# Performance work log

Measured on AMD Instinct MI355X. Metric: run time of the kernel, lower is better.

## Reference

```python
import jax, jax.numpy as jnp
import numpy as np

N = 50000      # neurons
R = 4          # receptors per neuron
D = 5          # max delay steps
N_IN = 17400   # input (LGN) channels
B = 2
T = 50
E_REC = 2000000
E_IN = 500000
DT = 1.0
SIGMA = 0.5    # gauss_std
DAMP = 0.3     # dampening_factor


@jax.custom_vjp
def spike_gauss(v):
    return (v > 0).astype(v.dtype)

def _sg_fwd(v):
    return (v > 0).astype(v.dtype), v

def _sg_bwd(v, g):
    return (g * jnp.exp(-(v * v) / (SIGMA * SIGMA)) * DAMP,)

spike_gauss.defvjp(_sg_fwd, _sg_bwd)


def _constrained(w):
    # Dale's law: sign buffer is fixed (stop_gradient), values clipped to keep sign
    s = jax.lax.stop_gradient(jnp.sign(w))
    return jnp.where(s >= 0, jax.nn.relu(w), -jax.nn.relu(-w))


def setup_inputs() -> dict:
    ks = jax.random.split(jax.random.key(0), 20)
    x = jax.random.uniform(ks[0], (B, T, N_IN), jnp.float32)
    rest = jax.random.randint(ks[1], (T, B), 0, 11).astype(jnp.int32)  # Binomial(10,0.1) count
    rec_rows = jax.random.randint(ks[2], (E_REC,), 0, R * N).astype(jnp.int32)
    rec_cols = jax.random.randint(ks[3], (E_REC,), 0, D * N).astype(jnp.int32)
    rec_w = jax.random.normal(ks[4], (E_REC,), jnp.float32) * 1e-3
    in_rows = jax.random.randint(ks[5], (E_IN,), 0, R * N).astype(jnp.int32)
    in_cols = jax.random.randint(ks[6], (E_IN,), 0, N_IN).astype(jnp.int32)
    in_w = jax.random.normal(ks[7], (E_IN,), jnp.float32) * 1e-3
    bkg = jax.random.normal(ks[8], (N * R,), jnp.float32) * 0.1
    # per-neuron params, already in normalized voltage units (offset=E_L, scale=V_th-E_L)
    v_th = jnp.ones((N,), jnp.float32)
    e_l = jnp.zeros((N,), jnp.float32)
    v_reset = jax.random.uniform(ks[9], (N,), jnp.float32, -0.2, 0.0)
    g = jax.random.uniform(ks[10], (N,), jnp.float32, 4.0, 6.0)
    c_m = jax.random.uniform(ks[11], (N,), jnp.float32, 100.0, 200.0)
    tau = c_m / g
    decay = jnp.exp(-DT / tau)
    current_factor = (1.0 - decay) * tau / c_m
    t_ref = jnp.full((N,), 2.0, jnp.float32)
    asc_amps = jax.random.normal(ks[12], (N, 2), jnp.float32) * 0.01
    param_k = jax.random.uniform(ks[13], (N, 2), jnp.float32, 0.1, 0.5)
    tau_syn = jax.random.uniform(ks[14], (N, R), jnp.float32, 2.0, 10.0)
    syn_decay = jnp.exp(-DT / tau_syn)
    psc_initial = jnp.asarray(np.e, jnp.float32) / tau_syn
    voltage_scale = jax.random.uniform(ks[15], (N,), jnp.float32, 20.0, 30.0)
    voltage_offset = jnp.full((N,), -70.0, jnp.float32)
    return dict(x=x, rec_w=rec_w, in_w=in_w, bkg=bkg, v_th=v_th, e_l=e_l,
                v_reset=v_reset, g=g, t_ref=t_ref, asc_amps=asc_amps,
                param_k=param_k, decay=decay, current_factor=current_factor,
                syn_decay=syn_decay, psc_initial=psc_initial,
                voltage_scale=voltage_scale, voltage_offset=voltage_offset,
                rec_rows=rec_rows, rec_cols=rec_cols, in_rows=in_rows,
                in_cols=in_cols, rest=rest)


def _forward(x, rec_w, in_w, bkg, v_th, e_l, v_reset, g, t_ref, asc_amps,
             param_k, decay, current_factor, syn_decay, psc_initial,
             voltage_scale, voltage_offset, rec_rows, rec_cols, in_rows,
             in_cols, rest):
    rec_wc = _constrained(rec_w)
    in_wc = _constrained(in_w)
    asc_decay = jnp.exp(-DT * param_k)   # (N,2)
    leak = g * e_l                       # (N,)
    normalizer = v_th - e_l              # (N,)

    z_buf0 = jnp.zeros((B, D, N), jnp.float32)  # delay line, slot 0 = most recent
    v0 = jnp.broadcast_to(v_reset, (B, N))
    zN = jnp.zeros((B, N), jnp.float32)
    zNR = jnp.zeros((B, N, R), jnp.float32)
    carry0 = (z_buf0, v0, zN, zN, zN, zNR, zNR)

    xs = (jnp.transpose(x, (1, 0, 2)), rest)  # (T,B,N_IN), (T,B)

    def step(carry, inp):
        x_t, rest_t = inp
        z_buf, v, r, a1, a2, psc_rise, psc = carry
        # input projection: sparse COO (R*N, N_IN) matvec per batch via gather + scatter-add
        cur = jnp.zeros((B, R * N), jnp.float32).at[:, in_rows].add(x_t[:, in_cols] * in_wc[None, :])
        cur = cur + bkg[None, :] * (rest_t.astype(jnp.float32)[:, None] / 10.0)
        prev_z = z_buf[:, 0]
        zb_flat = z_buf.reshape(B, D * N)
        # recurrent sparse COO (R*N, D*N) matvec over the delay buffer
        i_rec = jnp.zeros((B, R * N), jnp.float32).at[:, rec_rows].add(zb_flat[:, rec_cols] * rec_wc[None, :])
        rec_in = (i_rec + cur).reshape(B, N, R)
        new_psc_rise = syn_decay[None] * psc_rise + rec_in * psc_initial[None]
        new_psc = psc * syn_decay[None] + DT * syn_decay[None] * psc_rise
        new_r = jax.nn.relu(r + prev_z * t_ref[None] - DT)
        new_a1 = asc_decay[:, 0][None] * a1 + prev_z * asc_amps[:, 0][None]
        new_a2 = asc_decay[:, 1][None] * a2 + prev_z * asc_amps[:, 1][None]
        reset_current = prev_z * (v_reset - v_th)[None]
        input_current = psc.sum(-1)  # uses OLD psc, matching the torch code
        new_v = decay[None] * v + current_factor[None] * (input_current + a1 + a2 + leak[None]) + reset_current
        v_sc = (new_v - v_th[None]) / normalizer[None]
        new_z = spike_gauss(v_sc)
        new_z = jnp.where(new_r > 0.0, jnp.zeros_like(new_z), new_z)
        new_z_buf = jnp.concatenate([new_z[:, None, :], z_buf[:, :-1]], axis=1)
        v_out = new_v * voltage_scale[None] + voltage_offset[None]
        new_carry = (new_z_buf, new_v, new_r, new_a1, new_a2, new_psc_rise, new_psc)
        return new_carry, (new_z, v_out)

    _, (zs, vs) = jax.lax.scan(step, carry0, xs)
    return jnp.transpose(zs, (1, 0, 2)), jnp.transpose(vs, (1, 0, 2))  # (B,T,N) each


def reference(x, rec_w, in_w, bkg, v_th, e_l, v_reset, g, t_ref, asc_amps,
              param_k, decay, current_factor, syn_decay, psc_initial,
              voltage_scale, voltage_offset, rec_rows, rec_cols, in_rows,
              in_cols, rest):
    return _forward(x, rec_w, in_w, bkg, v_th, e_l, v_reset, g, t_ref,
                    asc_amps, param_k, decay, current_factor, syn_decay,
                    psc_initial, voltage_scale, voltage_offset, rec_rows,
                    rec_cols, in_rows, in_cols, rest)
```

## Files before the change

kernel.cpp:

```cpp
#include <hip/hip_runtime.h>
#include <hip/hip_cooperative_groups.h>

namespace cg = cooperative_groups;

#define NN    50000
#define RR    4
#define DDEP  5
#define NIN   17400
#define BB    2
#define TT    50
#define EREC  2000000
#define EIN   500000
#define RNN   (RR*NN)
#define DNN   (DDEP*NN)
#define RING  6
#define TB    (TT*BB)
#define CH    20
#define NCH   (TB/CH)
#define SCAN_TPB 256
#define SCAN_ITEMS 4

struct SP {
  const float* x; const float* bkg;
  const float* v_th; const float* e_l; const float* v_reset; const float* g;
  const float* t_ref; const float* asc_amps; const float* param_k;
  const float* decay; const float* cf; const float* syn_decay; const float* psc_init;
  const float* vscale; const float* voff;
  const int* rest;
  float* out_z; float* out_v;
  float* cur_ring;
  int*   flags;
  int*   bar;
  const int* row_ptr;
  const int2* cw_in;
  const int* col_ptr;
  const int2* cw_rec;
  const float* in_cur;
};

__global__ void hist2_k(const int* __restrict__ in_rows, const int* __restrict__ rec_cols,
                        int* __restrict__ cnt_in, int* __restrict__ cnt_rec) {
  int i = blockIdx.x * blockDim.x + threadIdx.x;
  int nth = gridDim.x * blockDim.x;
  for (int e = i; e < EIN + EREC; e += nth) {
    if (e < EIN) atomicAdd(&cnt_in[in_rows[e]], 1);
    else         atomicAdd(&cnt_rec[rec_cols[e - EIN]], 1);
  }
}

__global__ __launch_bounds__(SCAN_TPB) void blocksum_k(const int* __restrict__ cnt, int n,
                                                       int* __restrict__ partial) {
  __shared__ int sm[SCAN_TPB];
  int base = (blockIdx.x * SCAN_TPB + threadIdx.x) * SCAN_ITEMS;
  int s = 0;
  #pragma unroll
  for (int j = 0; j < SCAN_ITEMS; ++j) { int idx = base + j; if (idx < n) s += cnt[idx]; }
  sm[threadIdx.x] = s; __syncthreads();
  for (int off = SCAN_TPB / 2; off > 0; off >>= 1) {
    if (threadIdx.x < off) sm[threadIdx.x] += sm[threadIdx.x + off];
    __syncthreads();
  }
  if (threadIdx.x == 0) partial[blockIdx.x] = sm[0];
}

__global__ __launch_bounds__(SCAN_TPB) void scanpart_k(int* __restrict__ partial, int nb) {
  __shared__ int sm[SCAN_TPB];
  int i = threadIdx.x;
  int v = (i < nb) ? partial[i] : 0;
  sm[i] = v; __syncthreads();
  for (int off = 1; off < SCAN_TPB; off <<= 1) {
    int a = (i >= off) ? sm[i - off] : 0;
    __syncthreads();
    sm[i] += a;
    __syncthreads();
  }
  if (i < nb) partial[i] = sm[i] - v;
}

__global__ __launch_bounds__(SCAN_TPB) void finalize_k(const int* __restrict__ cnt, int n,
                                                       const int* __restrict__ partial,
                                                       int* __restrict__ ptr,
                                                       int* __restrict__ cursor, int nE) {
  __shared__ int sm[SCAN_TPB];
  int tidl = threadIdx.x;
  int base = (blockIdx.x * SCAN_TPB + tidl) * SCAN_ITEMS;
  int local[SCAN_ITEMS];
  int s = 0;
  #pragma unroll
  for (int j = 0; j < SCAN_ITEMS; ++j) {
    int idx = base + j;
    int c = (idx < n) ? cnt[idx] : 0;
    local[j] = c; s += c;
  }
  sm[tidl] = s; __syncthreads();
  for (int off = 1; off < SCAN_TPB; off <<= 1) {
    int a = (tidl >= off) ? sm[tidl - off] : 0;
    __syncthreads();
    sm[tidl] += a;
    __syncthreads();
  }
  int run = partial[blockIdx.x] + sm[tidl] - s;
  #pragma unroll
  for (int j = 0; j < SCAN_ITEMS; ++j) {
    int idx = base + j;
    if (idx < n) { ptr[idx] = run; cursor[idx] = run; run += local[j]; }
  }
  if (blockIdx.x == 0 && tidl == 0) ptr[n] = nE;
}

__global__ void scatter2_k(const int* __restrict__ in_rows, const int* __restrict__ in_cols,
                           const float* __restrict__ in_w,
                           const int* __restrict__ rec_cols, const int* __restrict__ rec_rows,
                           const float* __restrict__ rec_w,
                           int* __restrict__ cur_in, int* __restrict__ cur_rec,
                           int2* __restrict__ cw_in, int2* __restrict__ cw_rec) {
  int i = blockIdx.x * blockDim.x + threadIdx.x;
  int nth = gridDim.x * blockDim.x;
  for (int e = i; e < EIN + EREC; e += nth) {
    if (e < EIN) {
      int pos = atomicAdd(&cur_in[in_rows[e]], 1);
      cw_in[pos] = make_int2(in_cols[e], __float_as_int(in_w[e]));
    } else {
      int ee = e - EIN;
      int pos = atomicAdd(&cur_rec[rec_cols[ee]], 1);
      cw_rec[pos] = make_int2(rec_rows[ee], __float_as_int(rec_w[ee]));
    }
  }
}

__global__ __launch_bounds__(256) void xpose_k(const float* __restrict__ x,
                                               float* __restrict__ xT) {
  __shared__ float tile[64][TB + 1];
  int c0 = blockIdx.x * 64;
  int cl = threadIdx.x & 63;
  for (int tb = threadIdx.x >> 6; tb < TB; tb += 4) {
    int t = tb >> 1, b = tb & 1;
    int c = c0 + cl;
    tile[cl][tb] = (c < NIN) ? x[((size_t)b * TT + t) * NIN + c] : 0.f;
  }
  __syncthreads();
  int cc = threadIdx.x >> 2;
  int seg = (threadIdx.x & 3) * (TB / 4);
  int c = c0 + cc;
  if (c < NIN) {
    for (int j = seg; j < seg + TB / 4; ++j)
      xT[(size_t)c * TB + j] = tile[cc][j];
  }
}

__global__ __launch_bounds__(256) void precomp2_k(const float* __restrict__ xT,
                                                  const int* __restrict__ rest,
                                                  const float* __restrict__ bkg,
                                                  const int* __restrict__ row_ptr,
                                                  const int2* __restrict__ cw,
                                                  float* __restrict__ ic) {
  const int nbn = (NN + 255) >> 8;
  int chunk = blockIdx.x / nbn;
  int n = (blockIdx.x % nbn) * 256 + threadIdx.x;
  if (n >= NN) return;
  const int tb0 = chunk * CH;

  float restf[CH];
  #pragma unroll
  for (int j = 0; j < CH; ++j) restf[j] = (float)rest[tb0 + j] * 0.1f;

  int rp[RR + 1];
  #pragma unroll
  for (int r = 0; r <= RR; ++r) rp[r] = row_ptr[n * RR + r];

  float acc[RR][CH];
  #pragma unroll
  for (int r = 0; r < RR; ++r) {
    float bk = bkg[n * RR + r];
    #pragma unroll
    for (int j = 0; j < CH; ++j) acc[r][j] = bk * restf[j];
    for (int e = rp[r]; e < rp[r + 1]; ++e) {
      int2 c = cw[e];
      float w = __int_as_float(c.y);
      const float* xr = xT + (size_t)c.x * TB + tb0;
      #pragma unroll
      for (int j = 0; j < CH; ++j) acc[r][j] += w * xr[j];
    }
  }
  #pragma unroll
  for (int j = 0; j < CH; ++j) {
    *(float4*)(ic + (size_t)(tb0 + j) * RNN + (size_t)n * RR) =
        make_float4(acc[0][j], acc[1][j], acc[2][j], acc[3][j]);
  }
}

__device__ __forceinline__ void gridbar(int* bar, int nb, int target) {
  __syncthreads();
  if (threadIdx.x == 0) {
    int* cnt = bar;
    int* gen = bar + 32;
    int old = __hip_atomic_fetch_add(cnt, 1, __ATOMIC_ACQ_REL, __HIP_MEMORY_SCOPE_AGENT);
    if (old == nb - 1) {
      __hip_atomic_store(cnt, 0, __ATOMIC_RELAXED, __HIP_MEMORY_SCOPE_AGENT);
      __hip_atomic_store(gen, target, __ATOMIC_RELEASE, __HIP_MEMORY_SCOPE_AGENT);
    } else {
      while (__hip_atomic_load(gen, __ATOMIC_RELAXED, __HIP_MEMORY_SCOPE_AGENT) < target)
        __builtin_amdgcn_s_sleep(2);
      (void)__hip_atomic_load(gen, __ATOMIC_ACQUIRE, __HIP_MEMORY_SCOPE_AGENT);
    }
  }
  __syncthreads();
}

__global__ __launch_bounds__(1024, 1) void snn_all(SP p) {
  const int tid = blockIdx.x * blockDim.x + threadIdx.x;
  const int nb = gridDim.x;

  const bool owner = tid < BB * NN;
  int b = 0, n = 0;
  float sd[RR], pi[RR], bkgv[RR], psc_rise[RR], psc[RR];
  int rbeg[RR], rend[RR];
  float v = 0.f, refr = 0.f, a1 = 0.f, a2 = 0.f, my_z = 0.f;
  float dcy = 0.f, cfac = 0.f, trf = 0.f, amp1 = 0.f, amp2 = 0.f;
  float ad1 = 0.f, ad2 = 0.f, vth = 0.f, invn = 0.f, leak = 0.f;
  float vrst = 0.f, vsc = 0.f, vof = 0.f;
  #pragma unroll
  for (int r = 0; r < RR; ++r) {
    sd[r]=0.f; pi[r]=0.f; bkgv[r]=0.f; psc_rise[r]=0.f; psc[r]=0.f;
    rbeg[r]=0; rend[r]=0;
  }

  if (owner) {
    b = (tid >= NN) ? 1 : 0;
    n = tid - b * NN;
    #pragma unroll
    for (int r = 0; r < RR; ++r) {
      sd[r] = p.syn_decay[n*RR + r];
      pi[r] = p.psc_init[n*RR + r];
    }
    if (!p.in_cur) {
      #pragma unroll
      for (int r = 0; r < RR; ++r) {
        bkgv[r] = p.bkg[n*RR + r];
        rbeg[r] = p.row_ptr[n*RR + r];
        rend[r] = p.row_ptr[n*RR + r + 1];
      }
    }
    vth  = p.v_th[n];
    float el = p.e_l[n];
    invn = 1.0f / (vth - el);
    leak = p.g[n] * el;
    vrst = p.v_reset[n];
    v    = vrst;
    dcy  = p.decay[n];
    cfac = p.cf[n];
    trf  = p.t_ref[n];
    amp1 = p.asc_amps[2*n+0];
    amp2 = p.asc_amps[2*n+1];
    ad1  = expf(-p.param_k[2*n+0]);
    ad2  = expf(-p.param_k[2*n+1]);
    vsc  = p.vscale[n];
    vof  = p.voff[n];
  }
  const float* xb = p.x + (size_t)b * TT * NIN;
  float* ringB = p.cur_ring + (size_t)b * RING * RNN;

  float4 iv = make_float4(0.f, 0.f, 0.f, 0.f);
  if (owner && p.in_cur)
    iv = *(const float4*)(p.in_cur + (size_t)b * RNN + (size_t)n * RR);

  for (int t = 0; t < TT; ++t) {
    if (t) gridbar(p.bar, nb, t);

    if (owner) {
      int slot = t % RING;
      float rin[RR];

      if (p.in_cur) {
        rin[0] = iv.x; rin[1] = iv.y; rin[2] = iv.z; rin[3] = iv.w;
      } else {
        float restf = (float)p.rest[t*BB + b] * 0.1f;
        const float* xt = xb + (size_t)t * NIN;
        #pragma unroll
        for (int r = 0; r < RR; ++r) {
          float acc = bkgv[r] * restf;
          for (int e = rbeg[r]; e < rend[r]; ++e) {
            int2 cw = p.cw_in[e];
            acc += xt[cw.x] * __int_as_float(cw.y);
          }
          rin[r] = acc;
        }
      }

      if (p.flags[b*RING + slot] == t) {
        float4* slotR = (float4*)(ringB + (size_t)slot * RNN);
        float4 rv = slotR[n];
        slotR[n] = make_float4(0.f, 0.f, 0.f, 0.f);
        rin[0] += rv.x; rin[1] += rv.y; rin[2] += rv.z; rin[3] += rv.w;
      }

      float prev_z = my_z;
      float input_current = psc[0] + psc[1] + psc[2] + psc[3];
      float new_v = dcy * v + cfac * (input_current + a1 + a2 + leak)
                    + prev_z * (vrst - vth);
      #pragma unroll
      for (int r = 0; r < RR; ++r) {
        float npsc = psc[r] * sd[r] + sd[r] * psc_rise[r];
        psc_rise[r] = sd[r] * psc_rise[r] + rin[r] * pi[r];
        psc[r] = npsc;
      }
      refr = fmaxf(refr + prev_z * trf - 1.0f, 0.f);
      a1 = ad1 * a1 + prev_z * amp1;
      a2 = ad2 * a2 + prev_z * amp2;
      v = new_v;
      float v_scaled = (new_v - vth) * invn;
      float z = (v_scaled > 0.f) ? 1.f : 0.f;
      if (refr > 0.f) z = 0.f;
      my_z = z;
      size_t oidx = (size_t)b * (TT*NN) + (size_t)t * NN + n;
      p.out_z[oidx] = z;
      p.out_v[oidx] = new_v * vsc + vof;

      if (z != 0.f) {
        #pragma unroll
        for (int d = 0; d < DDEP; ++d) {
          int tt = t + 1 + d;
          if (tt >= TT) break;
          int col = d * NN + n;
          int be = p.col_ptr[col], en = p.col_ptr[col + 1];
          if (be != en) {
            int ws_ = tt % RING;
            p.flags[b*RING + ws_] = tt;
            float* ringW = ringB + (size_t)ws_ * RNN;
            for (int e = be; e < en; ++e) {
              int2 cw = p.cw_rec[e];
              atomicAdd(&ringW[cw.x], __int_as_float(cw.y));
            }
          }
        }
      }

      if (p.in_cur && t + 1 < TT)
        iv = *(const float4*)(p.in_cur + (size_t)((t+1)*BB + b) * RNN + (size_t)n * RR);
    }
  }
}

extern "C" void kernel_launch(void* const* d_in, const int* in_sizes, int n_in,
                              void* d_out, int out_size, void* d_ws, size_t ws_size,
                              hipStream_t stream) {
  SP p;
  p.x        = (const float*)d_in[0];
  const float* rec_w = (const float*)d_in[1];
  const float* in_w  = (const float*)d_in[2];
  p.bkg      = (const float*)d_in[3];
  p.v_th     = (const float*)d_in[4];
  p.e_l      = (const float*)d_in[5];
  p.v_reset  = (const float*)d_in[6];
  p.g        = (const float*)d_in[7];
  p.t_ref    = (const float*)d_in[8];
  p.asc_amps = (const float*)d_in[9];
  p.param_k  = (const float*)d_in[10];
  p.decay    = (const float*)d_in[11];
  p.cf       = (const float*)d_in[12];
  p.syn_decay= (const float*)d_in[13];
  p.psc_init = (const float*)d_in[14];
  p.vscale   = (const float*)d_in[15];
  p.voff     = (const float*)d_in[16];
  const int* rec_rows = (const int*)d_in[17];
  const int* rec_cols = (const int*)d_in[18];
  const int* in_rows  = (const int*)d_in[19];
  const int* in_cols  = (const int*)d_in[20];
  p.rest     = (const int*)d_in[21];
  p.out_z = (float*)d_out;
  p.out_v = (float*)d_out + (size_t)BB * TT * NN;

  char* ws = (char*)d_ws;
  size_t off = 0;
  auto alloc = [&](size_t bytes) { void* q = ws + off; off += (bytes + 255) & ~(size_t)255; return q; };
  float* cur_ring = (float*)alloc(sizeof(float) * (size_t)BB * RING * RNN);
  int*   flags    = (int*)  alloc(sizeof(int) * BB * RING);
  int*   bar      = (int*)  alloc(sizeof(int) * 64);
  int*   row_ptr  = (int*)  alloc(sizeof(int) * ((size_t)RNN + 1));
  int*   col_ptr  = (int*)  alloc(sizeof(int) * ((size_t)DNN + 1));
  int*   cnt_in   = (int*)  alloc(sizeof(int) * (size_t)RNN);
  int*   cnt_rec  = (int*)  alloc(sizeof(int) * (size_t)DNN);
  int*   cur_in   = (int*)  alloc(sizeof(int) * (size_t)RNN);
  int*   cur_rec  = (int*)  alloc(sizeof(int) * (size_t)DNN);
  int*   part_in  = (int*)  alloc(sizeof(int) * SCAN_TPB);
  int*   part_rec = (int*)  alloc(sizeof(int) * SCAN_TPB);
  int2*  cw_in    = (int2*) alloc(sizeof(int2) * (size_t)EIN);
  int2*  cw_rec   = (int2*) alloc(sizeof(int2) * (size_t)EREC);
  float* xT       = (float*)alloc(sizeof(float) * (size_t)NIN * TB);
  float* in_cur   = (float*)alloc(sizeof(float) * (size_t)TB * RNN);
  const bool use_pre = (off <= ws_size);

  p.cur_ring = cur_ring; p.flags = flags; p.bar = bar;
  p.row_ptr = row_ptr; p.cw_in = cw_in;
  p.col_ptr = col_ptr; p.cw_rec = cw_rec;
  p.in_cur = use_pre ? in_cur : nullptr;

  hipMemsetAsync(cur_ring, 0, sizeof(float) * (size_t)BB * RING * RNN, stream);
  hipMemsetAsync(flags, 0xFF, sizeof(int) * BB * RING, stream);
  hipMemsetAsync(bar, 0, sizeof(int) * 64, stream);
  hipMemsetAsync(cnt_in, 0, sizeof(int) * (size_t)RNN, stream);
  hipMemsetAsync(cnt_rec, 0, sizeof(int) * (size_t)DNN, stream);

  hipLaunchKernelGGL(hist2_k, dim3(1024), dim3(256), 0, stream,
                     in_rows, rec_cols, cnt_in, cnt_rec);

  const int NB_IN  = (RNN + SCAN_TPB * SCAN_ITEMS - 1) / (SCAN_TPB * SCAN_ITEMS);
  const int NB_REC = (DNN + SCAN_TPB * SCAN_ITEMS - 1) / (SCAN_TPB * SCAN_ITEMS);
  hipLaunchKernelGGL(blocksum_k, dim3(NB_IN),  dim3(SCAN_TPB), 0, stream, cnt_in,  RNN, part_in);
  hipLaunchKernelGGL(blocksum_k, dim3(NB_REC), dim3(SCAN_TPB), 0, stream, cnt_rec, DNN, part_rec);
  hipLaunchKernelGGL(scanpart_k, dim3(1), dim3(SCAN_TPB), 0, stream, part_in,  NB_IN);
  hipLaunchKernelGGL(scanpart_k, dim3(1), dim3(SCAN_TPB), 0, stream, part_rec, NB_REC);
  hipLaunchKernelGGL(finalize_k, dim3(NB_IN),  dim3(SCAN_TPB), 0, stream, cnt_in,  RNN, part_in,  row_ptr, cur_in,  EIN);
  hipLaunchKernelGGL(finalize_k, dim3(NB_REC), dim3(SCAN_TPB), 0, stream, cnt_rec, DNN, part_rec, col_ptr, cur_rec, EREC);

  hipLaunchKernelGGL(scatter2_k, dim3(1024), dim3(256), 0, stream,
                     in_rows, in_cols, in_w, rec_cols, rec_rows, rec_w,
                     cur_in, cur_rec, cw_in, cw_rec);

  if (use_pre) {
    hipLaunchKernelGGL(xpose_k, dim3((NIN + 63) / 64), dim3(256), 0, stream, p.x, xT);
    const int nbn = (NN + 255) / 256;
    hipLaunchKernelGGL(precomp2_k, dim3(nbn * NCH), dim3(256), 0, stream,
                       xT, p.rest, p.bkg, row_ptr, cw_in, in_cur);
  }

  void* args[] = { (void*)&p };
  hipLaunchCooperativeKernel(reinterpret_cast<const void*>(&snn_all),
                             dim3(104), dim3(1024), args, 0u, stream);
}
```

Baseline: 835.1 us.

## Overlap input-current precompute with recurrent scan using helper blocks and tree barrier

Removes the separate precompute kernel and moves its work into the persistent cooperative kernel. Blocks beyond the first 98 act as helpers: they compute the first 20 time-batch slices before the first grid barrier, then compute two slices per step ahead of the owner blocks. The grid grows to 256 blocks and the flat grid barrier becomes a two-level tree barrier, which reduces contention on a single counter. The ring-slot flags are dropped in favour of an unconditional read-and-clear, the scan kernels are merged into paired launches, and the memsets are coalesced into one. The risks are a larger cooperative grid, extra traffic competing with the latency-bound step loop, and a barrier that now has more participants.

```diff
diff --git a/kernel.cpp b/kernel.cpp
--- a/kernel.cpp
+++ b/kernel.cpp
@@ -1,7 +1,4 @@
 #include <hip/hip_runtime.h>
-#include <hip/hip_cooperative_groups.h>
-
-namespace cg = cooperative_groups;
 
 #define NN    50000
 #define RR    4
@@ -15,8 +12,13 @@
 #define DNN   (DDEP*NN)
 #define RING  6
 #define TB    (TT*BB)
-#define CH    20
-#define NCH   (TB/CH)
+#define NBLK  256
+#define TPB   1024
+#define OWNER_BLKS 98
+#define NHELP ((NBLK-OWNER_BLKS)*TPB)
+#define GRP   16
+#define NGRP  (NBLK/GRP)
+#define PRE_SLICES 20
 #define SCAN_TPB 256
 #define SCAN_ITEMS 4
 
@@ -29,13 +31,14 @@
   const int* rest;
   float* out_z; float* out_v;
   float* cur_ring;
-  int*   flags;
   int*   bar;
   const int* row_ptr;
   const int2* cw_in;
   const int* col_ptr;
   const int2* cw_rec;
-  const float* in_cur;
+  const float* xT;
+  float* ic;
+  int    use_pre;
 };
 
 __global__ void hist2_k(const int* __restrict__ in_rows, const int* __restrict__ rec_cols,
@@ -48,8 +51,15 @@
   }
 }
 
-__global__ __launch_bounds__(SCAN_TPB) void blocksum_k(const int* __restrict__ cnt, int n,
-                                                       int* __restrict__ partial) {
+__global__ __launch_bounds__(SCAN_TPB) void blocksum2_k(const int* __restrict__ cnt_in,
+                                                        const int* __restrict__ cnt_rec,
+                                                        int* __restrict__ part_in,
+                                                        int* __restrict__ part_rec) {
+  const int n = blockIdx.y ? DNN : RNN;
+  const int* cnt = blockIdx.y ? cnt_rec : cnt_in;
+  int* partial = blockIdx.y ? part_rec : part_in;
+  const int nb = (n + SCAN_TPB * SCAN_ITEMS - 1) / (SCAN_TPB * SCAN_ITEMS);
+  if ((int)blockIdx.x >= nb) return;
   __shared__ int sm[SCAN_TPB];
   int base = (blockIdx.x * SCAN_TPB + threadIdx.x) * SCAN_ITEMS;
   int s = 0;
@@ -63,7 +73,11 @@
   if (threadIdx.x == 0) partial[blockIdx.x] = sm[0];
 }
 
-__global__ __launch_bounds__(SCAN_TPB) void scanpart_k(int* __restrict__ partial, int nb) {
+__global__ __launch_bounds__(SCAN_TPB) void scanpart2_k(int* __restrict__ part_in,
+                                                        int* __restrict__ part_rec) {
+  const int n = blockIdx.x ? DNN : RNN;
+  int* partial = blockIdx.x ? part_rec : part_in;
+  const int nb = (n + SCAN_TPB * SCAN_ITEMS - 1) / (SCAN_TPB * SCAN_ITEMS);
   __shared__ int sm[SCAN_TPB];
   int i = threadIdx.x;
   int v = (i < nb) ? partial[i] : 0;
@@ -77,10 +91,22 @@
   if (i < nb) partial[i] = sm[i] - v;
 }
 
-__global__ __launch_bounds__(SCAN_TPB) void finalize_k(const int* __restrict__ cnt, int n,
-                                                       const int* __restrict__ partial,
-                                                       int* __restrict__ ptr,
-                                                       int* __restrict__ cursor, int nE) {
+__global__ __launch_bounds__(SCAN_TPB) void finalize2_k(const int* __restrict__ cnt_in,
+                                                        const int* __restrict__ cnt_rec,
+                                                        const int* __restrict__ part_in,
+                                                        const int* __restrict__ part_rec,
+                                                        int* __restrict__ ptr_in,
+                                                        int* __restrict__ ptr_rec,
+                                                        int* __restrict__ cur_in,
+                                                        int* __restrict__ cur_rec) {
+  const int n = blockIdx.y ? DNN : RNN;
+  const int nE = blockIdx.y ? EREC : EIN;
+  const int* cnt = blockIdx.y ? cnt_rec : cnt_in;
+  const int* partial = blockIdx.y ? part_rec : part_in;
+  int* ptr = blockIdx.y ? ptr_rec : ptr_in;
+  int* cursor = blockIdx.y ? cur_rec : cur_in;
+  const int nb = (n + SCAN_TPB * SCAN_ITEMS - 1) / (SCAN_TPB * SCAN_ITEMS);
+  if ((int)blockIdx.x >= nb) return;
   __shared__ int sm[SCAN_TPB];
   int tidl = threadIdx.x;
   int base = (blockIdx.x * SCAN_TPB + tidl) * SCAN_ITEMS;
@@ -148,70 +174,53 @@
   }
 }
 
-__global__ __launch_bounds__(256) void precomp2_k(const float* __restrict__ xT,
-                                                  const int* __restrict__ rest,
-                                                  const float* __restrict__ bkg,
-                                                  const int* __restrict__ row_ptr,
-                                                  const int2* __restrict__ cw,
-                                                  float* __restrict__ ic) {
-  const int nbn = (NN + 255) >> 8;
-  int chunk = blockIdx.x / nbn;
-  int n = (blockIdx.x % nbn) * 256 + threadIdx.x;
-  if (n >= NN) return;
-  const int tb0 = chunk * CH;
-
-  float restf[CH];
-  #pragma unroll
-  for (int j = 0; j < CH; ++j) restf[j] = (float)rest[tb0 + j] * 0.1f;
-
-  int rp[RR + 1];
-  #pragma unroll
-  for (int r = 0; r <= RR; ++r) rp[r] = row_ptr[n * RR + r];
-
-  float acc[RR][CH];
-  #pragma unroll
-  for (int r = 0; r < RR; ++r) {
-    float bk = bkg[n * RR + r];
-    #pragma unroll
-    for (int j = 0; j < CH; ++j) acc[r][j] = bk * restf[j];
-    for (int e = rp[r]; e < rp[r + 1]; ++e) {
-      int2 c = cw[e];
-      float w = __int_as_float(c.y);
-      const float* xr = xT + (size_t)c.x * TB + tb0;
-      #pragma unroll
-      for (int j = 0; j < CH; ++j) acc[r][j] += w * xr[j];
-    }
-  }
-  #pragma unroll
-  for (int j = 0; j < CH; ++j) {
-    *(float4*)(ic + (size_t)(tb0 + j) * RNN + (size_t)n * RR) =
-        make_float4(acc[0][j], acc[1][j], acc[2][j], acc[3][j]);
-  }
-}
-
-__device__ __forceinline__ void gridbar(int* bar, int nb, int target) {
+__device__ __forceinline__ void gridbar(int* bar, int target) {
   __syncthreads();
   if (threadIdx.x == 0) {
-    int* cnt = bar;
-    int* gen = bar + 32;
-    int old = __hip_atomic_fetch_add(cnt, 1, __ATOMIC_ACQ_REL, __HIP_MEMORY_SCOPE_AGENT);
-    if (old == nb - 1) {
-      __hip_atomic_store(cnt, 0, __ATOMIC_RELAXED, __HIP_MEMORY_SCOPE_AGENT);
-      __hip_atomic_store(gen, target, __ATOMIC_RELEASE, __HIP_MEMORY_SCOPE_AGENT);
+    int* leaf = bar + (blockIdx.x / GRP) * 32;
+    int* rootGen = bar + NGRP * 32;
+    int* rootCnt = rootGen + 32;
+    int lo = __hip_atomic_fetch_add(leaf, 1, __ATOMIC_ACQ_REL, __HIP_MEMORY_SCOPE_AGENT);
+    if (lo == GRP - 1) {
+      __hip_atomic_store(leaf, 0, __ATOMIC_RELAXED, __HIP_MEMORY_SCOPE_AGENT);
+      int ro = __hip_atomic_fetch_add(rootCnt, 1, __ATOMIC_ACQ_REL, __HIP_MEMORY_SCOPE_AGENT);
+      if (ro == NGRP - 1) {
+        __hip_atomic_store(rootCnt, 0, __ATOMIC_RELAXED, __HIP_MEMORY_SCOPE_AGENT);
+        __hip_atomic_store(rootGen, target, __ATOMIC_RELEASE, __HIP_MEMORY_SCOPE_AGENT);
+      } else {
+        while (__hip_atomic_load(rootGen, __ATOMIC_RELAXED, __HIP_MEMORY_SCOPE_AGENT) < target)
+          __builtin_amdgcn_s_sleep(2);
+        (void)__hip_atomic_load(rootGen, __ATOMIC_ACQUIRE, __HIP_MEMORY_SCOPE_AGENT);
+      }
     } else {
-      while (__hip_atomic_load(gen, __ATOMIC_RELAXED, __HIP_MEMORY_SCOPE_AGENT) < target)
+      while (__hip_atomic_load(rootGen, __ATOMIC_RELAXED, __HIP_MEMORY_SCOPE_AGENT) < target)
         __builtin_amdgcn_s_sleep(2);
-      (void)__hip_atomic_load(gen, __ATOMIC_ACQUIRE, __HIP_MEMORY_SCOPE_AGENT);
+      (void)__hip_atomic_load(rootGen, __ATOMIC_ACQUIRE, __HIP_MEMORY_SCOPE_AGENT);
     }
   }
   __syncthreads();
 }
 
-__global__ __launch_bounds__(1024, 1) void snn_all(SP p) {
-  const int tid = blockIdx.x * blockDim.x + threadIdx.x;
-  const int nb = gridDim.x;
-
-  const bool owner = tid < BB * NN;
+__device__ __forceinline__ void helper_item(const SP& p, int n, int s) {
+  float restf = (float)p.rest[s] * 0.1f;
+  const int* rp = p.row_ptr + n * RR;
+  int r0 = rp[0], r1 = rp[1], r2 = rp[2], r3 = rp[3], r4 = rp[4];
+  float4 bk = *(const float4*)(p.bkg + (size_t)n * RR);
+  float a0 = bk.x * restf, a1 = bk.y * restf, a2 = bk.z * restf, a3 = bk.w * restf;
+  const float* xs = p.xT + s;
+  for (int e = r0; e < r1; ++e) { int2 c = p.cw_in[e]; a0 += __int_as_float(c.y) * xs[(size_t)c.x * TB]; }
+  for (int e = r1; e < r2; ++e) { int2 c = p.cw_in[e]; a1 += __int_as_float(c.y) * xs[(size_t)c.x * TB]; }
+  for (int e = r2; e < r3; ++e) { int2 c = p.cw_in[e]; a2 += __int_as_float(c.y) * xs[(size_t)c.x * TB]; }
+  for (int e = r3; e < r4; ++e) { int2 c = p.cw_in[e]; a3 += __int_as_float(c.y) * xs[(size_t)c.x * TB]; }
+  *(float4*)(p.ic + (size_t)s * RNN + (size_t)n * RR) = make_float4(a0, a1, a2, a3);
+}
+
+__global__ __launch_bounds__(TPB, 1) void snn_all(SP p) {
+  const int tid = blockIdx.x * TPB + threadIdx.x;
+  const bool hblk = blockIdx.x >= OWNER_BLKS;
+  const int hr = hblk ? (blockIdx.x - OWNER_BLKS) * TPB + threadIdx.x : 0;
+
+  const bool owner = !hblk && tid < BB * NN;
   int b = 0, n = 0;
   float sd[RR], pi[RR], bkgv[RR], psc_rise[RR], psc[RR];
   int rbeg[RR], rend[RR];
@@ -233,7 +242,7 @@
       sd[r] = p.syn_decay[n*RR + r];
       pi[r] = p.psc_init[n*RR + r];
     }
-    if (!p.in_cur) {
+    if (!p.use_pre) {
       #pragma unroll
       for (int r = 0; r < RR; ++r) {
         bkgv[r] = p.bkg[n*RR + r];
@@ -260,18 +269,24 @@
   const float* xb = p.x + (size_t)b * TT * NIN;
   float* ringB = p.cur_ring + (size_t)b * RING * RNN;
 
+  if (hblk && p.use_pre) {
+    for (int w = hr; w < PRE_SLICES * NN; w += NHELP) {
+      int s = w / NN;
+      helper_item(p, w - s * NN, s);
+    }
+  }
+  gridbar(p.bar, 1);
+
   float4 iv = make_float4(0.f, 0.f, 0.f, 0.f);
-  if (owner && p.in_cur)
-    iv = *(const float4*)(p.in_cur + (size_t)b * RNN + (size_t)n * RR);
+  if (owner && p.use_pre)
+    iv = *(const float4*)(p.ic + (size_t)b * RNN + (size_t)n * RR);
 
   for (int t = 0; t < TT; ++t) {
-    if (t) gridbar(p.bar, nb, t);
+    if (t) gridbar(p.bar, t + 1);
 
     if (owner) {
-      int slot = t % RING;
       float rin[RR];
-
-      if (p.in_cur) {
+      if (p.use_pre) {
         rin[0] = iv.x; rin[1] = iv.y; rin[2] = iv.z; rin[3] = iv.w;
       } else {
         float restf = (float)p.rest[t*BB + b] * 0.1f;
@@ -287,8 +302,8 @@
         }
       }
 
-      if (p.flags[b*RING + slot] == t) {
-        float4* slotR = (float4*)(ringB + (size_t)slot * RNN);
+      {
+        float4* slotR = (float4*)(ringB + (size_t)(t % RING) * RNN);
         float4 rv = slotR[n];
         slotR[n] = make_float4(0.f, 0.f, 0.f, 0.f);
         rin[0] += rv.x; rin[1] += rv.y; rin[2] += rv.z; rin[3] += rv.w;
@@ -324,9 +339,7 @@
           int col = d * NN + n;
           int be = p.col_ptr[col], en = p.col_ptr[col + 1];
           if (be != en) {
-            int ws_ = tt % RING;
-            p.flags[b*RING + ws_] = tt;
-            float* ringW = ringB + (size_t)ws_ * RNN;
+            float* ringW = ringB + (size_t)(tt % RING) * RNN;
             for (int e = be; e < en; ++e) {
               int2 cw = p.cw_rec[e];
               atomicAdd(&ringW[cw.x], __int_as_float(cw.y));
@@ -335,8 +348,16 @@
         }
       }
 
-      if (p.in_cur && t + 1 < TT)
-        iv = *(const float4*)(p.in_cur + (size_t)((t+1)*BB + b) * RNN + (size_t)n * RR);
+      if (p.use_pre && t + 1 < TT)
+        iv = *(const float4*)(p.ic + (size_t)((t+1)*BB + b) * RNN + (size_t)n * RR);
+    } else if (hblk && p.use_pre) {
+      int s0 = PRE_SLICES + 2 * t;
+      if (s0 < TB) {
+        for (int w = hr; w < 2 * NN; w += NHELP) {
+          int s = s0 + (w >= NN);
+          if (s < TB) helper_item(p, (w >= NN) ? w - NN : w, s);
+        }
+      }
     }
   }
 }
@@ -374,12 +395,12 @@
   size_t off = 0;
   auto alloc = [&](size_t bytes) { void* q = ws + off; off += (bytes + 255) & ~(size_t)255; return q; };
   float* cur_ring = (float*)alloc(sizeof(float) * (size_t)BB * RING * RNN);
-  int*   flags    = (int*)  alloc(sizeof(int) * BB * RING);
-  int*   bar      = (int*)  alloc(sizeof(int) * 64);
+  int*   bar      = (int*)  alloc(4096);
+  int*   cnt_in   = (int*)  alloc(sizeof(int) * (size_t)RNN);
+  int*   cnt_rec  = (int*)  alloc(sizeof(int) * (size_t)DNN);
+  size_t zero_end = off;
   int*   row_ptr  = (int*)  alloc(sizeof(int) * ((size_t)RNN + 1));
   int*   col_ptr  = (int*)  alloc(sizeof(int) * ((size_t)DNN + 1));
-  int*   cnt_in   = (int*)  alloc(sizeof(int) * (size_t)RNN);
-  int*   cnt_rec  = (int*)  alloc(sizeof(int) * (size_t)DNN);
   int*   cur_in   = (int*)  alloc(sizeof(int) * (size_t)RNN);
   int*   cur_rec  = (int*)  alloc(sizeof(int) * (size_t)DNN);
   int*   part_in  = (int*)  alloc(sizeof(int) * SCAN_TPB);
@@ -390,28 +411,24 @@
   float* in_cur   = (float*)alloc(sizeof(float) * (size_t)TB * RNN);
   const bool use_pre = (off <= ws_size);
 
-  p.cur_ring = cur_ring; p.flags = flags; p.bar = bar;
+  p.cur_ring = bar ? cur_ring : cur_ring; p.cur_ring = cur_ring; p.bar = bar;
   p.row_ptr = row_ptr; p.cw_in = cw_in;
   p.col_ptr = col_ptr; p.cw_rec = cw_rec;
-  p.in_cur = use_pre ? in_cur : nullptr;
+  p.xT = xT; p.ic = in_cur;
+  p.use_pre = use_pre ? 1 : 0;
 
   hipMemsetAsync(cur_ring, 0, sizeof(float) * (size_t)BB * RING * RNN, stream);
-  hipMemsetAsync(flags, 0xFF, sizeof(int) * BB * RING, stream);
-  hipMemsetAsync(bar, 0, sizeof(int) * 64, stream);
-  hipMemsetAsync(cnt_in, 0, sizeof(int) * (size_t)RNN, stream);
-  hipMemsetAsync(cnt_rec, 0, sizeof(int) * (size_t)DNN, stream);
+  hipMemsetAsync(bar, 0, zero_end - ((char*)bar - ws), stream);
 
   hipLaunchKernelGGL(hist2_k, dim3(1024), dim3(256), 0, stream,
                      in_rows, rec_cols, cnt_in, cnt_rec);
 
-  const int NB_IN  = (RNN + SCAN_TPB * SCAN_ITEMS - 1) / (SCAN_TPB * SCAN_ITEMS);
   const int NB_REC = (DNN + SCAN_TPB * SCAN_ITEMS - 1) / (SCAN_TPB * SCAN_ITEMS);
-  hipLaunchKernelGGL(blocksum_k, dim3(NB_IN),  dim3(SCAN_TPB), 0, stream, cnt_in,  RNN, part_in);
-  hipLaunchKernelGGL(blocksum_k, dim3(NB_REC), dim3(SCAN_TPB), 0, stream, cnt_rec, DNN, part_rec);
-  hipLaunchKernelGGL(scanpart_k, dim3(1), dim3(SCAN_TPB), 0, stream, part_in,  NB_IN);
-  hipLaunchKernelGGL(scanpart_k, dim3(1), dim3(SCAN_TPB), 0, stream, part_rec, NB_REC);
-  hipLaunchKernelGGL(finalize_k, dim3(NB_IN),  dim3(SCAN_TPB), 0, stream, cnt_in,  RNN, part_in,  row_ptr, cur_in,  EIN);
-  hipLaunchKernelGGL(finalize_k, dim3(NB_REC), dim3(SCAN_TPB), 0, stream, cnt_rec, DNN, part_rec, col_ptr, cur_rec, EREC);
+  hipLaunchKernelGGL(blocksum2_k, dim3(NB_REC, 2), dim3(SCAN_TPB), 0, stream,
+                     cnt_in, cnt_rec, part_in, part_rec);
+  hipLaunchKernelGGL(scanpart2_k, dim3(2), dim3(SCAN_TPB), 0, stream, part_in, part_rec);
+  hipLaunchKernelGGL(finalize2_k, dim3(NB_REC, 2), dim3(SCAN_TPB), 0, stream,
+                     cnt_in, cnt_rec, part_in, part_rec, row_ptr, col_ptr, cur_in, cur_rec);
 
   hipLaunchKernelGGL(scatter2_k, dim3(1024), dim3(256), 0, stream,
                      in_rows, in_cols, in_w, rec_cols, rec_rows, rec_w,
@@ -419,12 +436,9 @@
 
   if (use_pre) {
     hipLaunchKernelGGL(xpose_k, dim3((NIN + 63) / 64), dim3(256), 0, stream, p.x, xT);
-    const int nbn = (NN + 255) / 256;
-    hipLaunchKernelGGL(precomp2_k, dim3(nbn * NCH), dim3(256), 0, stream,
-                       xT, p.rest, p.bkg, row_ptr, cw_in, in_cur);
   }
 
   void* args[] = { (void*)&p };
   hipLaunchCooperativeKernel(reinterpret_cast<const void*>(&snn_all),
-                             dim3(104), dim3(1024), args, 0u, stream);
-}
+                             dim3(NBLK), dim3(TPB), args, 0u, stream);
+}
```

Measured after the change: 1.928 ms. +130.9%, slower.
